# Optimization experiments

Measured on AMD Instinct MI355X. Metric: run time of the kernel, lower is better.

## Reference

```python
import jax, jax.numpy as jnp
import numpy as np

DIM = 1024
N_HEADS = 16
HEAD_DIM = DIM // N_HEADS
SCALE = HEAD_DIM ** -0.5


def setup_inputs() -> dict:
    key = jax.random.key(0)
    ks = jax.random.split(key, 10)
    B, L, L_low = 4, 4096, 1024
    s = DIM ** -0.5
    return {
        "x_broad": jax.random.normal(ks[0], (B, L, DIM), jnp.float32),
        "x_low": jax.random.normal(ks[1], (B, L_low, DIM), jnp.float32),
        "Wq": jax.random.normal(ks[2], (DIM, DIM), jnp.float32) * s,
        "bq": jnp.zeros((DIM,), jnp.float32),
        "Wk": jax.random.normal(ks[3], (DIM, DIM), jnp.float32) * s,
        "bk": jnp.zeros((DIM,), jnp.float32),
        "Wv": jax.random.normal(ks[4], (DIM, DIM), jnp.float32) * s,
        "bv": jnp.zeros((DIM,), jnp.float32),
        "Wo": jax.random.normal(ks[5], (DIM, DIM), jnp.float32) * s,
        "bo": jnp.zeros((DIM,), jnp.float32),
    }


def reference(x_broad, x_low, Wq, bq, Wk, bk, Wv, bv, Wo, bo):
    B, L, D = x_broad.shape
    Ll = x_low.shape[1]
    # projections (torch Linear: x @ W.T + b)
    q = (x_broad @ Wq.T + bq).reshape(B, L, N_HEADS, HEAD_DIM)
    k = (x_low @ Wk.T + bk).reshape(B, Ll, N_HEADS, HEAD_DIM)
    v = (x_low @ Wv.T + bv).reshape(B, Ll, N_HEADS, HEAD_DIM)
    # scores: [B, H, L, L_low]
    attn = jnp.einsum("blhd,bmhd->bhlm", q, k) * SCALE
    attn = jax.nn.softmax(attn, axis=-1)
    out = jnp.einsum("bhlm,bmhd->blhd", attn, v).reshape(B, L, D)
    return out @ Wo.T + bo
```

## Files before the change

### kernel.cpp

```cpp
#include <hip/hip_runtime.h>
#include <hip/hip_bf16.h>

typedef __bf16 bf16;
typedef __bf16 bf16x4 __attribute__((ext_vector_type(4)));
typedef __bf16 bf16x8 __attribute__((ext_vector_type(8)));
typedef float f32x4 __attribute__((ext_vector_type(4)));

#define MFMA16(a, b, c) __builtin_amdgcn_mfma_f32_16x16x32_bf16(a, b, c, 0, 0, 0)

constexpr int DIM = 1024;
constexpr int NH = 16;
constexpr int HD = 64;
constexpr float SCALE = 0.125f;
constexpr float L2E = 1.4426950408889634f;
constexpr float SCL2E = SCALE * L2E;

constexpr int ilog2(int v) {
  int s = 0;
  while ((1 << s) < v) ++s;
  return s;
}

__device__ __forceinline__ float fast_exp2(float x) {
  float r;
  asm("v_exp_f32 %0, %1" : "=v"(r) : "v"(x));
  return r;
}

__device__ __forceinline__ void gl_lds16(const void* g, void* l) {
  __builtin_amdgcn_global_load_lds((const __attribute__((address_space(1))) void*)g,
                                   (__attribute__((address_space(3))) void*)l, 16, 0, 0);
}

__global__ __launch_bounds__(256) void cvt_f32_bf16(const float* __restrict__ s,
                                                    bf16* __restrict__ d, int n8) {
  const int i = blockIdx.x * 256 + threadIdx.x;
  if (i < n8) {
    const float4 v0 = ((const float4*)s)[i * 2];
    const float4 v1 = ((const float4*)s)[i * 2 + 1];
    bf16x8 o = {(bf16)v0.x, (bf16)v0.y, (bf16)v0.z, (bf16)v0.w,
                (bf16)v1.x, (bf16)v1.y, (bf16)v1.z, (bf16)v1.w};
    ((bf16x8*)d)[i] = o;
  }
}

__global__ __launch_bounds__(256) void cvt_w4(const float* __restrict__ a,
                                              const float* __restrict__ b,
                                              const float* __restrict__ c,
                                              const float* __restrict__ d,
                                              bf16* __restrict__ o) {
  constexpr int N8 = DIM * DIM / 8;
  const int i = blockIdx.x * 256 + threadIdx.x;
  const int g = i >> 17;
  const int j = i & (N8 - 1);
  const float* s = (g == 0) ? a : (g == 1) ? b : (g == 2) ? c : d;
  const float4 v0 = ((const float4*)s)[j * 2];
  const float4 v1 = ((const float4*)s)[j * 2 + 1];
  bf16x8 ov = {(bf16)v0.x, (bf16)v0.y, (bf16)v0.z, (bf16)v0.w,
               (bf16)v1.x, (bf16)v1.y, (bf16)v1.z, (bf16)v1.w};
  ((bf16x8*)o)[i] = ov;
}

template <int OUT_MODE, int LQ>
__global__ __launch_bounds__(512) void gemm_big(const bf16* __restrict__ A,
                                                const bf16* __restrict__ W,
                                                const float* __restrict__ bias,
                                                void* __restrict__ Cptr,
                                                float oscale) {
  constexpr int LQS = ilog2(LQ);
  __shared__ bf16 Ls[3][2][256 * 32];

  const int bm = blockIdx.x * 256;
  const int bn = blockIdx.y * 256;
  const int tid = threadIdx.x;
  const int w = tid >> 6;
  const int lane = tid & 63;
  const int quad = lane >> 4;
  const int l16 = lane & 15;
  const int wr = w >> 1;
  const int wc = w & 1;
  const int lr4 = lane >> 2;
  const int c4 = ((lane & 3) ^ (lr4 & 3)) << 3;

  int aS[2], bS[2];
#pragma unroll
  for (int i = 0; i < 2; ++i) {
    const int rr = (i * 8 + w) * 16 + lr4;
    aS[i] = (bm + rr) * DIM + c4;
    bS[i] = (bn + rr) * DIM + c4;
  }

  auto stage = [&](int t, int bi) {
#pragma unroll
    for (int i = 0; i < 2; ++i) {
      gl_lds16(A + aS[i] + t * 32, (char*)&Ls[bi][0][0] + (i * 8 + w) * 1024);
      gl_lds16(W + bS[i] + t * 32, (char*)&Ls[bi][1][0] + (i * 8 + w) * 1024);
    }
  };

  f32x4 acc[8][4] = {};

  const int rowBase = wr * 64;
  const int colBase = wc * 128;

  stage(0, 0);
  stage(1, 1);

  int bi = 0;
  for (int t = 0; t < 32; ++t) {
    if (t < 31)
      asm volatile("s_waitcnt vmcnt(4)" ::: "memory");
    else
      asm volatile("s_waitcnt vmcnt(0)" ::: "memory");
    __builtin_amdgcn_s_barrier();
    __builtin_amdgcn_sched_barrier(0);

    if (t + 2 < 32) stage(t + 2, bi == 0 ? 2 : bi - 1);

    const char* baseA = (const char*)&Ls[bi][0][0];
    const char* baseB = (const char*)&Ls[bi][1][0];
    const int sw = ((quad ^ (l16 & 3)) << 4);

    bf16x8 af[4], bfr[8];
#pragma unroll
    for (int mi = 0; mi < 4; ++mi)
      af[mi] = *(const bf16x8*)(baseA + (rowBase + mi * 16 + l16) * 64 + sw);
#pragma unroll
    for (int ni = 0; ni < 8; ++ni)
      bfr[ni] = *(const bf16x8*)(baseB + (colBase + ni * 16 + l16) * 64 + sw);

    __builtin_amdgcn_s_setprio(1);
#pragma unroll
    for (int ni = 0; ni < 8; ++ni)
#pragma unroll
      for (int mi = 0; mi < 4; ++mi)
        acc[ni][mi] = MFMA16(af[mi], bfr[ni], acc[ni][mi]);
    __builtin_amdgcn_s_setprio(0);

    bi = (bi == 2) ? 0 : bi + 1;
  }

  float bcol[8];
#pragma unroll
  for (int ni = 0; ni < 8; ++ni) bcol[ni] = bias[bn + colBase + ni * 16 + l16];

#pragma unroll
  for (int ni = 0; ni < 8; ++ni) {
    const int col = bn + colBase + ni * 16 + l16;
#pragma unroll
    for (int mi = 0; mi < 4; ++mi) {
#pragma unroll
      for (int r = 0; r < 4; ++r) {
        const int row = bm + rowBase + mi * 16 + quad * 4 + r;
        const float val = (acc[ni][mi][r] + bcol[ni]) * oscale;
        if constexpr (OUT_MODE == 0) {
          ((float*)Cptr)[(size_t)row * DIM + col] = val;
        } else {
          const int b = row >> LQS;
          const int l = row & (LQ - 1);
          ((bf16*)Cptr)[((((size_t)(b * NH + (col >> 6)) << LQS) + l) << 6) +
                        (col & 63)] = (bf16)val;
        }
      }
    }
  }
}

template <int OUT_MODE, int LQ>
__global__ __launch_bounds__(256) void gemm_bf16(const bf16* __restrict__ A,
                                                 const bf16* __restrict__ W,
                                                 const float* __restrict__ bias,
                                                 void* __restrict__ Cptr,
                                                 float oscale) {
  constexpr int LQS = ilog2(LQ);
  __shared__ bf16 As[128 * 64];
  __shared__ bf16 Bs[128 * 64];

  const int bm = blockIdx.x * 128;
  const int bn = blockIdx.y * 128;
  const int tid = threadIdx.x;
  const int w = tid >> 6;
  const int lane = tid & 63;
  const int quad = lane >> 4;
  const int l16 = lane & 15;
  const int wm = (w >> 1) * 64;
  const int wn = (w & 1) * 64;
  const int lr = lane >> 3;
  const int sc8 = (((lane & 7) ^ lr)) << 3;
  const int x7 = l16 & 7;

  size_t aOff[4], bOff[4];
#pragma unroll
  for (int r = 0; r < 4; ++r) {
    const int rowt = (r * 4 + w) * 8 + lr;
    aOff[r] = (size_t)(bm + rowt) * DIM + sc8;
    bOff[r] = (size_t)(bn + rowt) * DIM + sc8;
  }

  f32x4 acc[4][4] = {};

  for (int k0 = 0; k0 < DIM; k0 += 64) {
#pragma unroll
    for (int r = 0; r < 4; ++r) {
      gl_lds16(A + aOff[r] + k0, (char*)As + (r * 4 + w) * 1024);
      gl_lds16(W + bOff[r] + k0, (char*)Bs + (r * 4 + w) * 1024);
    }
    __syncthreads();

#pragma unroll
    for (int s = 0; s < 2; ++s) {
      bf16x8 af[4], bfr[4];
#pragma unroll
      for (int mi = 0; mi < 4; ++mi)
        af[mi] = *(const bf16x8*)((char*)As + (wm + mi * 16 + l16) * 128 +
                                  (((quad + 4 * s) ^ x7) << 4));
#pragma unroll
      for (int ni = 0; ni < 4; ++ni)
        bfr[ni] = *(const bf16x8*)((char*)Bs + (wn + ni * 16 + l16) * 128 +
                                   (((quad + 4 * s) ^ x7) << 4));
#pragma unroll
      for (int mi = 0; mi < 4; ++mi)
#pragma unroll
        for (int ni = 0; ni < 4; ++ni)
          acc[mi][ni] = MFMA16(af[mi], bfr[ni], acc[mi][ni]);
    }
    __syncthreads();
  }

  float bcol[4];
#pragma unroll
  for (int ni = 0; ni < 4; ++ni)
    bcol[ni] = (OUT_MODE == 3) ? 0.f : bias[bn + wn + ni * 16 + l16];

#pragma unroll
  for (int mi = 0; mi < 4; ++mi) {
    float brow[4];
    if constexpr (OUT_MODE == 3) {
#pragma unroll
      for (int r = 0; r < 4; ++r) brow[r] = bias[bm + wm + mi * 16 + quad * 4 + r];
    }
#pragma unroll
    for (int ni = 0; ni < 4; ++ni) {
      const int col = bn + wn + ni * 16 + l16;
#pragma unroll
      for (int r = 0; r < 4; ++r) {
        const int row = bm + wm + mi * 16 + quad * 4 + r;
        if constexpr (OUT_MODE == 0) {
          const float val = (acc[mi][ni][r] + bcol[ni]) * oscale;
          ((float*)Cptr)[(size_t)row * DIM + col] = val;
        } else if constexpr (OUT_MODE == 1) {
          const float val = (acc[mi][ni][r] + bcol[ni]) * oscale;
          const int b = row >> LQS;
          const int l = row & (LQ - 1);
          ((bf16*)Cptr)[((((size_t)(b * NH + (col >> 6)) << LQS) + l) << 6) +
                        (col & 63)] = (bf16)val;
        } else {
          const float val = acc[mi][ni][r] + brow[r];
          const int bb = col >> 10;
          const int kv = col & 1023;
          ((bf16*)Cptr)[((size_t)(bb * 1024 + row)) * 1024 + kv] = (bf16)val;
        }
      }
    }
  }
}

template <int OUT_MODE, bool A_BF16>
__global__ __launch_bounds__(256) void gemm_nt(const void* __restrict__ Aptr,
                                               const float* __restrict__ W,
                                               const float* __restrict__ bias,
                                               void* __restrict__ Cptr, int Lq,
                                               float oscale) {
  constexpr int LDT = 72;
  __shared__ bf16 As[128 * LDT];
  __shared__ bf16 Bs[128 * LDT];

  const int bm = blockIdx.x * 128;
  const int bn = blockIdx.y * 128;
  const int tid = threadIdx.x;
  const int w = tid >> 6;
  const int lane = tid & 63;
  const int quad = lane >> 4;
  const int l16 = lane & 15;
  const int wm = (w >> 1) * 64;
  const int wn = (w & 1) * 64;

  f32x4 acc[4][4] = {};

  for (int k0 = 0; k0 < DIM; k0 += 64) {
#pragma unroll
    for (int i = 0; i < 8; ++i) {
      int f = i * 256 + tid;
      int row = f >> 4;
      int c4 = (f & 15) << 2;
      const float4 v = *(const float4*)(W + (size_t)(bn + row) * DIM + k0 + c4);
      bf16x4 bv = {(bf16)v.x, (bf16)v.y, (bf16)v.z, (bf16)v.w};
      *(bf16x4*)&Bs[row * LDT + c4] = bv;
    }
    if constexpr (A_BF16) {
      const bf16* Ab = (const bf16*)Aptr;
#pragma unroll
      for (int i = 0; i < 4; ++i) {
        int f = i * 256 + tid;
        int row = f >> 3;
        int c8 = (f & 7) << 3;
        *(bf16x8*)&As[row * LDT + c8] =
            *(const bf16x8*)(Ab + (size_t)(bm + row) * DIM + k0 + c8);
      }
    } else {
      const float* Af = (const float*)Aptr;
#pragma unroll
      for (int i = 0; i < 8; ++i) {
        int f = i * 256 + tid;
        int row = f >> 4;
        int c4 = (f & 15) << 2;
        const float4 v = *(const float4*)(Af + (size_t)(bm + row) * DIM + k0 + c4);
        bf16x4 av = {(bf16)v.x, (bf16)v.y, (bf16)v.z, (bf16)v.w};
        *(bf16x4*)&As[row * LDT + c4] = av;
      }
    }
    __syncthreads();

#pragma unroll
    for (int sub = 0; sub < 2; ++sub) {
      bf16x8 af[4], bfr[4];
#pragma unroll
      for (int mi = 0; mi < 4; ++mi)
        af[mi] = *(const bf16x8*)&As[(wm + mi * 16 + l16) * LDT + sub * 32 + quad * 8];
#pragma unroll
      for (int ni = 0; ni < 4; ++ni)
        bfr[ni] = *(const bf16x8*)&Bs[(wn + ni * 16 + l16) * LDT + sub * 32 + quad * 8];
#pragma unroll
      for (int mi = 0; mi < 4; ++mi)
#pragma unroll
        for (int ni = 0; ni < 4; ++ni)
          acc[mi][ni] = MFMA16(af[mi], bfr[ni], acc[mi][ni]);
    }
    __syncthreads();
  }

#pragma unroll
  for (int mi = 0; mi < 4; ++mi) {
#pragma unroll
    for (int ni = 0; ni < 4; ++ni) {
      const int col = bn + wn + ni * 16 + l16;
      const float bv = bias[col];
#pragma unroll
      for (int r = 0; r < 4; ++r) {
        const int row = bm + wm + mi * 16 + quad * 4 + r;
        const float val = (acc[mi][ni][r] + bv) * oscale;
        if constexpr (OUT_MODE == 0) {
          ((float*)Cptr)[(size_t)row * DIM + col] = val;
        } else if constexpr (OUT_MODE == 1) {
          const int b = row / Lq;
          const int l = row - b * Lq;
          ((bf16*)Cptr)[((size_t)((b * NH + (col >> 6)) * Lq + l) << 6) + (col & 63)] =
              (bf16)val;
        } else {
          const int b = row >> 10;
          const int kv = row & 1023;
          ((bf16*)Cptr)[(((size_t)(b * NH + (col >> 6)) << 6) + (col & 63)) * 1024 + kv] =
              (bf16)val;
        }
      }
    }
  }
}

__global__ __launch_bounds__(256) void attn_fused(const bf16* __restrict__ Q,
                                                  const bf16* __restrict__ K,
                                                  const bf16* __restrict__ VT,
                                                  bf16* __restrict__ O) {
  __shared__ bf16 Ks[2][64 * 64];
  __shared__ bf16 Vs[2][64 * 64];
  __shared__ bf16 Ps[4 * 16 * 64];

  const int qt = blockIdx.x;
  const int h = blockIdx.y;
  const int b = blockIdx.z;
  const int tid = threadIdx.x;
  const int w = tid >> 6;
  const int lane = tid & 63;
  const int quad = lane >> 4;
  const int l16 = lane & 15;
  const int lr = lane >> 3;
  const int sc8 = (((lane & 7) ^ lr)) << 3;
  const int x7 = l16 & 7;

  const bf16* Qp = Q + ((size_t)(b * NH + h) * 4096 + qt * 128 + w * 32 + l16) * HD + quad * 8;
  const bf16* Kb = K + (size_t)(b * NH + h) * 1024 * HD;
  const bf16* Vb = VT + (size_t)(b * NH + h) * HD * 1024;

  bf16x8 qf[2][2];
#pragma unroll
  for (int g = 0; g < 2; ++g)
#pragma unroll
    for (int s = 0; s < 2; ++s) qf[g][s] = *(const bf16x8*)(Qp + g * 16 * HD + s * 32);

  char* pw = (char*)&Ps[w * 16 * 64];

  f32x4 oacc[2][4] = {};
  f32x4 lacc[2] = {};

  bf16x8 ones;
#pragma unroll
  for (int i = 0; i < 8; ++i) ones[i] = (bf16)1.0f;

  auto stage = [&](int kt, int bi) {
#pragma unroll
    for (int c2 = 0; c2 < 2; ++c2) {
      const int c = c2 * 4 + w;
      gl_lds16(Kb + (size_t)(kt + c * 8 + lr) * HD + sc8, (char*)&Ks[bi][0] + c * 1024);
      gl_lds16(Vb + (size_t)(c * 8 + lr) * 1024 + kt + sc8, (char*)&Vs[bi][0] + c * 1024);
    }
  };

  stage(0, 0);
  int buf = 0;
  for (int kt = 0; kt < 1024; kt += 64) {
    __syncthreads();
    if (kt + 64 < 1024) stage(kt + 64, buf ^ 1);

    bf16x8 kf[4][2];
#pragma unroll
    for (int nt = 0; nt < 4; ++nt)
#pragma unroll
      for (int s = 0; s < 2; ++s)
        kf[nt][s] = *(const bf16x8*)((char*)&Ks[buf][0] + (nt * 16 + l16) * 128 +
                                     (((quad + 4 * s) ^ x7) << 4));

    bf16x8 pf[2][2];
#pragma unroll
    for (int g = 0; g < 2; ++g) {
      __builtin_amdgcn_s_setprio(1);
#pragma unroll
      for (int nt = 0; nt < 4; ++nt) {
        f32x4 a = {0.f, 0.f, 0.f, 0.f};
        a = MFMA16(kf[nt][0], qf[g][0], a);
        a = MFMA16(kf[nt][1], qf[g][1], a);
        bf16x4 pb;
#pragma unroll
        for (int r = 0; r < 4; ++r) pb[r] = (bf16)fast_exp2(a[r]);
        *(bf16x4*)(pw + l16 * 128 + ((nt * 32 + quad * 8) ^ (x7 << 4))) = pb;
      }
      __builtin_amdgcn_s_setprio(0);
#pragma unroll
      for (int s = 0; s < 2; ++s)
        pf[g][s] = *(const bf16x8*)(pw + l16 * 128 + ((s * 64 + quad * 16) ^ (x7 << 4)));
      lacc[g] = MFMA16(ones, pf[g][0], lacc[g]);
      lacc[g] = MFMA16(ones, pf[g][1], lacc[g]);
    }

    __builtin_amdgcn_s_setprio(1);
#pragma unroll
    for (int dt = 0; dt < 4; ++dt) {
      bf16x8 vf0 = *(const bf16x8*)((char*)&Vs[buf][0] + (dt * 16 + l16) * 128 +
                                    ((quad ^ x7) << 4));
      bf16x8 vf1 = *(const bf16x8*)((char*)&Vs[buf][0] + (dt * 16 + l16) * 128 +
                                    ((((quad + 4)) ^ x7) << 4));
      oacc[0][dt] = MFMA16(vf0, pf[0][0], oacc[0][dt]);
      oacc[0][dt] = MFMA16(vf1, pf[0][1], oacc[0][dt]);
      oacc[1][dt] = MFMA16(vf0, pf[1][0], oacc[1][dt]);
      oacc[1][dt] = MFMA16(vf1, pf[1][1], oacc[1][dt]);
    }
    __builtin_amdgcn_s_setprio(0);
    buf ^= 1;
  }

  const float inv[2] = {1.f / lacc[0][0], 1.f / lacc[1][0]};

#pragma unroll
  for (int g = 0; g < 2; ++g) {
    const size_t orow =
        ((size_t)(b * 4096 + qt * 128 + w * 32 + g * 16 + l16)) * DIM + h * 64;
#pragma unroll
    for (int dt = 0; dt < 4; ++dt) {
      bf16x4 ov = {(bf16)(oacc[g][dt][0] * inv[g]), (bf16)(oacc[g][dt][1] * inv[g]),
                   (bf16)(oacc[g][dt][2] * inv[g]), (bf16)(oacc[g][dt][3] * inv[g])};
      *(bf16x4*)(O + orow + dt * 16 + quad * 4) = ov;
    }
  }
}

extern "C" void kernel_launch(void* const* d_in, const int* in_sizes, int n_in,
                              void* d_out, int out_size, void* d_ws, size_t ws_size,
                              hipStream_t stream) {
  const float* x_broad = (const float*)d_in[0];
  const float* x_low = (const float*)d_in[1];
  const float* Wq = (const float*)d_in[2];
  const float* bq = (const float*)d_in[3];
  const float* Wk = (const float*)d_in[4];
  const float* bk = (const float*)d_in[5];
  const float* Wv = (const float*)d_in[6];
  const float* bv = (const float*)d_in[7];
  const float* Wo = (const float*)d_in[8];
  const float* bo = (const float*)d_in[9];

  constexpr int B = 4, L = 4096, LL = 1024;
  const size_t qBytes = (size_t)B * NH * L * HD * 2;
  const size_t kvBytes = (size_t)B * NH * LL * HD * 2;
  const size_t oBytes = qBytes;
  const size_t xlBytes = kvBytes;
  const size_t wBytes = (size_t)DIM * DIM * 2;

  char* ws = (char*)d_ws;
  bf16* Qw = (bf16*)ws;
  bf16* Kw = (bf16*)(ws + qBytes);
  bf16* Vw = (bf16*)(ws + qBytes + kvBytes);
  bf16* Ow = (bf16*)(ws + qBytes + 2 * kvBytes);

  const dim3 blk(256);
  const size_t need = qBytes + 2 * kvBytes + oBytes + xlBytes + 4 * wBytes;

  if (ws_size >= need) {
    bf16* xbB = Ow;
    bf16* xlB = (bf16*)(ws + qBytes + 2 * kvBytes + oBytes);
    bf16* WqB = (bf16*)(ws + qBytes + 2 * kvBytes + oBytes + xlBytes);
    bf16* WkB = WqB + (size_t)DIM * DIM;
    bf16* WvB = WkB + (size_t)DIM * DIM;
    bf16* WoB = WvB + (size_t)DIM * DIM;

    hipLaunchKernelGGL(cvt_f32_bf16, dim3(B * L * DIM / 8 / 256), blk, 0, stream,
                       x_broad, xbB, B * L * DIM / 8);
    hipLaunchKernelGGL(cvt_f32_bf16, dim3(B * LL * DIM / 8 / 256), blk, 0, stream,
                       x_low, xlB, B * LL * DIM / 8);
    hipLaunchKernelGGL(cvt_w4, dim3(4 * DIM * DIM / 8 / 256), blk, 0, stream, Wq, Wk,
                       Wv, Wo, WqB);

    hipLaunchKernelGGL((gemm_big<1, L>), dim3(B * L / 256, DIM / 256), dim3(512), 0,
                       stream, xbB, WqB, bq, Qw, SCL2E);
    hipLaunchKernelGGL((gemm_bf16<1, LL>), dim3(B * LL / 128, DIM / 128), blk, 0,
                       stream, xlB, WkB, bk, Kw, 1.0f);
    hipLaunchKernelGGL((gemm_bf16<3, 1>), dim3(DIM / 128, B * LL / 128), blk, 0,
                       stream, WvB, xlB, bv, Vw, 1.0f);
    hipLaunchKernelGGL(attn_fused, dim3(L / 128, NH, B), blk, 0, stream, Qw, Kw, Vw, Ow);
    hipLaunchKernelGGL((gemm_big<0, 1>), dim3(B * L / 256, DIM / 256), dim3(512), 0,
                       stream, Ow, WoB, bo, d_out, 1.0f);
  } else {
    hipLaunchKernelGGL((gemm_nt<1, false>), dim3(B * L / 128, DIM / 128), blk, 0,
                       stream, x_broad, Wq, bq, Qw, L, SCL2E);
    hipLaunchKernelGGL((gemm_nt<1, false>), dim3(B * LL / 128, DIM / 128), blk, 0,
                       stream, x_low, Wk, bk, Kw, LL, 1.0f);
    hipLaunchKernelGGL((gemm_nt<2, false>), dim3(B * LL / 128, DIM / 128), blk, 0,
                       stream, x_low, Wv, bv, Vw, LL, 1.0f);
    hipLaunchKernelGGL(attn_fused, dim3(L / 128, NH, B), blk, 0, stream, Qw, Kw, Vw, Ow);
    hipLaunchKernelGGL((gemm_nt<0, true>), dim3(B * L / 128, DIM / 128), blk, 0,
                       stream, Ow, Wo, bo, d_out, 1, 1.0f);
  }
}
```

Measured before the change: 370.9 us.

## Restructure projection GEMM main loop with K=64 double-buffered tiles and interleaved LDS reads

Rewrites the big projection GEMM's main loop to take K=64 per iteration (two 32-wide halves) in a double buffer instead of a triple buffer of K=32 tiles. The 8 waves now form a 2x4 grid (128x64 per wave) instead of 4x2. Per-wave A-fragment LDS reads are split into four phases, each interleaved with MFMA groups, and the next global stage is issued mid-iteration. It also sets launch_bounds(512,2) to aim for two blocks per CU. The goal is fewer loop iterations and barriers per K and better overlap of LDS reads with MFMA. In exchange there are more intra-iteration barriers, and the larger LDS footprint (128KB) may prevent two blocks from actually co-residing.

After: 389.0 us. 4.9% more time.

```diff
diff --git a/kernel.cpp b/kernel.cpp
--- a/kernel.cpp
+++ b/kernel.cpp
@@ -62,13 +62,15 @@
 }
 
 template <int OUT_MODE, int LQ>
-__global__ __launch_bounds__(512) void gemm_big(const bf16* __restrict__ A,
-                                                const bf16* __restrict__ W,
-                                                const float* __restrict__ bias,
-                                                void* __restrict__ Cptr,
-                                                float oscale) {
+__global__ __launch_bounds__(512, 2) void gemm_big(const bf16* __restrict__ A,
+                                                   const bf16* __restrict__ W,
+                                                   const float* __restrict__ bias,
+                                                   void* __restrict__ Cptr,
+                                                   float oscale) {
   constexpr int LQS = ilog2(LQ);
-  __shared__ bf16 Ls[3][2][256 * 32];
+  constexpr int NT = DIM / 64;
+  __shared__ bf16 AS[2][2][256 * 32];
+  __shared__ bf16 BS[2][2][256 * 32];
 
   const int bm = blockIdx.x * 256;
   const int bn = blockIdx.y * 256;
@@ -77,78 +79,130 @@
   const int lane = tid & 63;
   const int quad = lane >> 4;
   const int l16 = lane & 15;
-  const int wr = w >> 1;
-  const int wc = w & 1;
   const int lr4 = lane >> 2;
-  const int c4 = ((lane & 3) ^ (lr4 & 3)) << 3;
-
-  int aS[2], bS[2];
-#pragma unroll
-  for (int i = 0; i < 2; ++i) {
-    const int rr = (i * 8 + w) * 16 + lr4;
-    aS[i] = (bm + rr) * DIM + c4;
-    bS[i] = (bn + rr) * DIM + c4;
-  }
-
-  auto stage = [&](int t, int bi) {
-#pragma unroll
-    for (int i = 0; i < 2; ++i) {
-      gl_lds16(A + aS[i] + t * 32, (char*)&Ls[bi][0][0] + (i * 8 + w) * 1024);
-      gl_lds16(W + bS[i] + t * 32, (char*)&Ls[bi][1][0] + (i * 8 + w) * 1024);
+  const int sc = ((lane & 3) ^ (lr4 & 3)) << 3;
+  const int rowBase = (w >> 2) * 128;
+  const int colBase = (w & 3) * 64;
+  const int swz = (quad ^ (l16 & 3)) << 4;
+
+  const size_t aRow = (size_t)(bm + w * 16 + lr4) * DIM + sc;
+  const size_t bRow = (size_t)(bn + w * 16 + lr4) * DIM + sc;
+
+  auto stage = [&](int t, int c) {
+#pragma unroll
+    for (int i = 0; i < 4; ++i) {
+      const int k = i >> 1, hf = i & 1;
+      const size_t off = (size_t)(hf * 128) * DIM + t * 64 + k * 32;
+      gl_lds16(A + aRow + off, (char*)&AS[c][k][0] + hf * 8192 + w * 1024);
+      gl_lds16(W + bRow + off, (char*)&BS[c][k][0] + hf * 8192 + w * 1024);
     }
   };
 
-  f32x4 acc[8][4] = {};
-
-  const int rowBase = wr * 64;
-  const int colBase = wc * 128;
+  f32x4 acc[4][8] = {};
 
   stage(0, 0);
   stage(1, 1);
-
-  int bi = 0;
-  for (int t = 0; t < 32; ++t) {
-    if (t < 31)
-      asm volatile("s_waitcnt vmcnt(4)" ::: "memory");
-    else
+  asm volatile("s_waitcnt vmcnt(8)" ::: "memory");
+  __builtin_amdgcn_s_barrier();
+
+  int c = 0;
+  for (int t = 0; t < NT; ++t) {
+    const char* A0 = (const char*)&AS[c][0][0];
+    const char* A1 = (const char*)&AS[c][1][0];
+    const char* B0 = (const char*)&BS[c][0][0];
+    const char* B1 = (const char*)&BS[c][1][0];
+    const int aB = (rowBase + l16) * 64 + swz;
+    const int bB = (colBase + l16) * 64 + swz;
+
+    bf16x8 bf0[4], bf1[4];
+#pragma unroll
+    for (int ni = 0; ni < 4; ++ni) {
+      bf0[ni] = *(const bf16x8*)(B0 + bB + ni * 1024);
+      bf1[ni] = *(const bf16x8*)(B1 + bB + ni * 1024);
+    }
+    bf16x8 a0k0 = *(const bf16x8*)(A0 + aB + 0 * 1024);
+    bf16x8 a0k1 = *(const bf16x8*)(A1 + aB + 0 * 1024);
+    bf16x8 a1k0 = *(const bf16x8*)(A0 + aB + 1 * 1024);
+    bf16x8 a1k1 = *(const bf16x8*)(A1 + aB + 1 * 1024);
+    __builtin_amdgcn_s_barrier();
+    asm volatile("s_waitcnt lgkmcnt(0)" ::: "memory");
+    __builtin_amdgcn_s_setprio(1);
+#pragma unroll
+    for (int ni = 0; ni < 4; ++ni) {
+      acc[ni][0] = MFMA16(a0k0, bf0[ni], acc[ni][0]);
+      acc[ni][0] = MFMA16(a0k1, bf1[ni], acc[ni][0]);
+      acc[ni][1] = MFMA16(a1k0, bf0[ni], acc[ni][1]);
+      acc[ni][1] = MFMA16(a1k1, bf1[ni], acc[ni][1]);
+    }
+    __builtin_amdgcn_s_setprio(0);
+
+    a0k0 = *(const bf16x8*)(A0 + aB + 2 * 1024);
+    a0k1 = *(const bf16x8*)(A1 + aB + 2 * 1024);
+    a1k0 = *(const bf16x8*)(A0 + aB + 3 * 1024);
+    a1k1 = *(const bf16x8*)(A1 + aB + 3 * 1024);
+    __builtin_amdgcn_s_barrier();
+    asm volatile("s_waitcnt lgkmcnt(0)" ::: "memory");
+    __builtin_amdgcn_s_setprio(1);
+#pragma unroll
+    for (int ni = 0; ni < 4; ++ni) {
+      acc[ni][2] = MFMA16(a0k0, bf0[ni], acc[ni][2]);
+      acc[ni][2] = MFMA16(a0k1, bf1[ni], acc[ni][2]);
+      acc[ni][3] = MFMA16(a1k0, bf0[ni], acc[ni][3]);
+      acc[ni][3] = MFMA16(a1k1, bf1[ni], acc[ni][3]);
+    }
+    __builtin_amdgcn_s_setprio(0);
+
+    a0k0 = *(const bf16x8*)(A0 + aB + 4 * 1024);
+    a0k1 = *(const bf16x8*)(A1 + aB + 4 * 1024);
+    a1k0 = *(const bf16x8*)(A0 + aB + 5 * 1024);
+    a1k1 = *(const bf16x8*)(A1 + aB + 5 * 1024);
+    __builtin_amdgcn_s_barrier();
+    asm volatile("s_waitcnt lgkmcnt(0)" ::: "memory");
+    __builtin_amdgcn_s_setprio(1);
+#pragma unroll
+    for (int ni = 0; ni < 4; ++ni) {
+      acc[ni][4] = MFMA16(a0k0, bf0[ni], acc[ni][4]);
+      acc[ni][4] = MFMA16(a0k1, bf1[ni], acc[ni][4]);
+      acc[ni][5] = MFMA16(a1k0, bf0[ni], acc[ni][5]);
+      acc[ni][5] = MFMA16(a1k1, bf1[ni], acc[ni][5]);
+    }
+    __builtin_amdgcn_s_setprio(0);
+
+    a0k0 = *(const bf16x8*)(A0 + aB + 6 * 1024);
+    a0k1 = *(const bf16x8*)(A1 + aB + 6 * 1024);
+    a1k0 = *(const bf16x8*)(A0 + aB + 7 * 1024);
+    a1k1 = *(const bf16x8*)(A1 + aB + 7 * 1024);
+    asm volatile("s_waitcnt lgkmcnt(0)" ::: "memory");
+    __builtin_amdgcn_s_barrier();
+    if (t + 2 < NT) stage(t + 2, c);
+    __builtin_amdgcn_s_setprio(1);
+#pragma unroll
+    for (int ni = 0; ni < 4; ++ni) {
+      acc[ni][6] = MFMA16(a0k0, bf0[ni], acc[ni][6]);
+      acc[ni][6] = MFMA16(a0k1, bf1[ni], acc[ni][6]);
+      acc[ni][7] = MFMA16(a1k0, bf0[ni], acc[ni][7]);
+      acc[ni][7] = MFMA16(a1k1, bf1[ni], acc[ni][7]);
+    }
+    __builtin_amdgcn_s_setprio(0);
+
+    if (t < NT - 2) {
+      asm volatile("s_waitcnt vmcnt(8)" ::: "memory");
+    } else if (t == NT - 2) {
       asm volatile("s_waitcnt vmcnt(0)" ::: "memory");
-    __builtin_amdgcn_s_barrier();
-    __builtin_amdgcn_sched_barrier(0);
-
-    if (t + 2 < 32) stage(t + 2, bi == 0 ? 2 : bi - 1);
-
-    const char* baseA = (const char*)&Ls[bi][0][0];
-    const char* baseB = (const char*)&Ls[bi][1][0];
-    const int sw = ((quad ^ (l16 & 3)) << 4);
-
-    bf16x8 af[4], bfr[8];
-#pragma unroll
-    for (int mi = 0; mi < 4; ++mi)
-      af[mi] = *(const bf16x8*)(baseA + (rowBase + mi * 16 + l16) * 64 + sw);
-#pragma unroll
-    for (int ni = 0; ni < 8; ++ni)
-      bfr[ni] = *(const bf16x8*)(baseB + (colBase + ni * 16 + l16) * 64 + sw);
-
-    __builtin_amdgcn_s_setprio(1);
-#pragma unroll
-    for (int ni = 0; ni < 8; ++ni)
-#pragma unroll
-      for (int mi = 0; mi < 4; ++mi)
-        acc[ni][mi] = MFMA16(af[mi], bfr[ni], acc[ni][mi]);
-    __builtin_amdgcn_s_setprio(0);
-
-    bi = (bi == 2) ? 0 : bi + 1;
-  }
-
-  float bcol[8];
-#pragma unroll
-  for (int ni = 0; ni < 8; ++ni) bcol[ni] = bias[bn + colBase + ni * 16 + l16];
-
-#pragma unroll
-  for (int ni = 0; ni < 8; ++ni) {
+    }
+    if (t < NT - 1) __builtin_amdgcn_s_barrier();
+    c ^= 1;
+  }
+
+  float bcol[4];
+#pragma unroll
+  for (int ni = 0; ni < 4; ++ni) bcol[ni] = bias[bn + colBase + ni * 16 + l16];
+
+#pragma unroll
+  for (int ni = 0; ni < 4; ++ni) {
     const int col = bn + colBase + ni * 16 + l16;
 #pragma unroll
-    for (int mi = 0; mi < 4; ++mi) {
+    for (int mi = 0; mi < 8; ++mi) {
 #pragma unroll
       for (int r = 0; r < 4; ++r) {
         const int row = bm + rowBase + mi * 16 + quad * 4 + r;
```
